# Optimization experiments

Measured on AMD Instinct MI355X. Metric: run time of the kernel, lower is better.

The kernel has to match this reference:

```python
import jax, jax.numpy as jnp
import numpy as np

B, T, C = 128, 256, 384
H, HD = 8, 48          # num_heads, head_dim
WINDOW = 64

def setup_inputs() -> dict:
    key = jax.random.key(0)
    ks = jax.random.split(key, 5)
    return {
        "x": jax.random.normal(ks[0], (B, T, C), dtype=jnp.float32),
        "W_qkv": jax.random.normal(ks[1], (C, 3 * C), dtype=jnp.float32) * (1.0 / np.sqrt(C)),
        "b_qkv": jax.random.normal(ks[2], (3 * C,), dtype=jnp.float32) * 0.02,
        "W_proj": jax.random.normal(ks[3], (C, C), dtype=jnp.float32) * (1.0 / np.sqrt(C)),
        "b_proj": jax.random.normal(ks[4], (C,), dtype=jnp.float32) * 0.02,
        "gate": jnp.ones((C,), dtype=jnp.float32),
    }

def reference(x, W_qkv, b_qkv, W_proj, b_proj, gate):
    Bx, Tx, Cx = x.shape
    qkv = x @ W_qkv + b_qkv                                   # [B,T,3C]
    q, k, v = jnp.split(qkv, 3, axis=-1)
    q = q.reshape(Bx, Tx, H, HD).transpose(0, 2, 1, 3)        # [B,H,T,hd]
    k = k.reshape(Bx, Tx, H, HD).transpose(0, 2, 1, 3)
    v = v.reshape(Bx, Tx, H, HD).transpose(0, 2, 1, 3)
    scale = 1.0 / np.sqrt(HD).astype(np.float32)
    att = jnp.einsum("bhqd,bhkd->bhqk", q, k) * scale        # [B,H,T,T]
    idx = jnp.arange(Tx)
    causal = idx[:, None] >= idx[None, :]                     # lower-tri
    local = jnp.abs(idx[None, :] - idx[:, None]) <= WINDOW
    mask = (causal & local)[None, None, :, :]
    att = jnp.where(mask, att, -jnp.inf)
    att = jax.nn.softmax(att, axis=-1)
    out = jnp.einsum("bhqk,bhkd->bhqd", att, v)               # [B,H,T,hd]
    out = out.transpose(0, 2, 1, 3).reshape(Bx, Tx, Cx)       # [B,T,C]
    return (out * gate) @ W_proj + b_proj
```

## Files before the change

### kernel.cpp

```cpp
#include <hip/hip_runtime.h>
#include <hip/hip_bf16.h>

typedef __attribute__((ext_vector_type(8))) short bf16x8;
typedef __attribute__((ext_vector_type(4))) float floatx4;

#define NB 128
#define NT 256
#define NC 384
#define NH 8
#define ND 48
#define CPLANE (128 * 8 * 256 * 48)

static __device__ __forceinline__ unsigned short f2bf(float f) {
  __hip_bfloat16 h = __float2bfloat16(f);
  return __builtin_bit_cast(unsigned short, h);
}

static __device__ __forceinline__ void gload16(const unsigned short* g, unsigned short* l) {
  __builtin_amdgcn_global_load_lds(
      (const __attribute__((address_space(1))) void*)g,
      (__attribute__((address_space(3))) void*)l, 16, 0, 0);
}

__global__ __launch_bounds__(256) void k_prep(const float* __restrict__ x,
                                              const float* __restrict__ Wq,
                                              const float* __restrict__ Wp,
                                              const float* __restrict__ gate,
                                              unsigned short* __restrict__ xbf,
                                              unsigned short* __restrict__ WqT,
                                              unsigned short* __restrict__ WpT) {
  const int blk = blockIdx.x;
  const int t = threadIdx.x;
  if (blk < 144) {
    __shared__ float T[64][65];
    const float* src;
    unsigned short* dst;
    int N, kt, nt;
    const bool isWp = (blk >= 108);
    if (!isWp) { src = Wq; dst = WqT; N = 1152; kt = blk / 18; nt = blk % 18; }
    else { int b2 = blk - 108; src = Wp; dst = WpT; N = 384; kt = b2 / 6; nt = b2 % 6; }
    const int k0 = kt * 64, n0 = nt * 64;
    const int r = t >> 2, c = (t & 3) * 16;
    const float* s = src + (size_t)(k0 + r) * N + n0 + c;
#pragma unroll
    for (int i = 0; i < 4; ++i) *(float4*)&T[r][c + i * 4] = ((const float4*)s)[i];
    __syncthreads();
    float gv[16];
    if (isWp) {
#pragma unroll
      for (int i = 0; i < 4; ++i) *(float4*)&gv[i * 4] = ((const float4*)(gate + k0 + c))[i];
    } else {
#pragma unroll
      for (int i = 0; i < 16; ++i) gv[i] = 1.f;
    }
    unsigned short o[16];
#pragma unroll
    for (int i = 0; i < 16; ++i) o[i] = f2bf(T[c + i][r] * gv[i]);
    unsigned short* dp = dst + (size_t)(n0 + r) * 384 + k0 + c;
    *(bf16x8*)dp = *(bf16x8*)&o[0];
    *(bf16x8*)(dp + 8) = *(bf16x8*)&o[8];
  } else {
    const int n8 = (NB * NT * NC) / 8;
    int idx = (blk - 144) * 256 + t;
    const int stride = (gridDim.x - 144) * 256;
    for (; idx < n8; idx += stride) {
      const float* s = x + (size_t)idx * 8;
      float v[8];
      *(float4*)&v[0] = ((const float4*)s)[0];
      *(float4*)&v[4] = ((const float4*)s)[1];
      bf16x8 p;
#pragma unroll
      for (int i = 0; i < 8; ++i) p[i] = f2bf(v[i]);
      *(bf16x8*)(xbf + (size_t)idx * 8) = p;
    }
  }
}

#define STAGE_G(Ag, Bg, k0, buf)                                                     \
  {                                                                                  \
    const int r0_ = (lane >> 2), sw0_ = 8 * ((lane & 3) ^ ((r0_ >> 1) & 3));         \
    const int r1_ = r0_ + 16,    sw1_ = 8 * ((lane & 3) ^ ((r1_ >> 1) & 3));         \
    gload16((Ag) + (size_t)r0_ * 384 + (k0) + sw0_, As + (buf)*4096 + (w * 32) * 32);  \
    gload16((Ag) + (size_t)r1_ * 384 + (k0) + sw1_, As + (buf)*4096 + (w * 32 + 16) * 32); \
    gload16((Bg) + (size_t)r0_ * 384 + (k0) + sw0_, Bs + (buf)*4096 + (w * 32) * 32);  \
    gload16((Bg) + (size_t)r1_ * 384 + (k0) + sw1_, Bs + (buf)*4096 + (w * 32 + 16) * 32); \
  }

#define GEMM_PIPE(Ag, Bg)                                                            \
  STAGE_G(Ag, Bg, 0, 0);                                                             \
  STAGE_G(Ag, Bg, 32, 1);                                                            \
  _Pragma("unroll") for (int t_ = 0; t_ < 12; ++t_) {                                \
    if (t_ < 11) asm volatile("s_waitcnt vmcnt(4)" ::: "memory");                    \
    else         asm volatile("s_waitcnt vmcnt(0)" ::: "memory");                    \
    __builtin_amdgcn_s_barrier();                                                    \
    if (t_ < 10) STAGE_G(Ag, Bg, (t_ + 2) * 32, (t_ + 2) % 3);                       \
    const unsigned short* Ac_ = As + (t_ % 3) * 4096;                                \
    const unsigned short* Bc_ = Bs + (t_ % 3) * 4096;                                \
    bf16x8 a_[4], b_[4];                                                             \
    _Pragma("unroll") for (int mt = 0; mt < 4; ++mt) {                               \
      const int R = wm * 64 + mt * 16 + lq;                                          \
      a_[mt] = *(const bf16x8*)&Ac_[R * 32 + 8 * (lg ^ ((R >> 1) & 3))];             \
    }                                                                                \
    _Pragma("unroll") for (int nt = 0; nt < 4; ++nt) {                               \
      const int R = wn * 64 + nt * 16 + lq;                                          \
      b_[nt] = *(const bf16x8*)&Bc_[R * 32 + 8 * (lg ^ ((R >> 1) & 3))];             \
    }                                                                                \
    _Pragma("unroll") for (int mt = 0; mt < 4; ++mt)                                 \
      _Pragma("unroll") for (int nt = 0; nt < 4; ++nt)                               \
        acc[mt][nt] = __builtin_amdgcn_mfma_f32_16x16x32_bf16(a_[mt], b_[nt], acc[mt][nt], 0, 0, 0); \
  }

__global__ __launch_bounds__(256) void k_qkv(const unsigned short* __restrict__ xb,
                                             const unsigned short* __restrict__ WqT,
                                             const float* __restrict__ bq,
                                             unsigned short* __restrict__ qkv) {
  __shared__ __align__(16) unsigned short As[3 * 4096];
  __shared__ __align__(16) unsigned short Bs[3 * 4096];
  const int t = threadIdx.x, lane = t & 63, w = t >> 6;
  const int wm = w >> 1, wn = w & 1;
  const int lq = lane & 15, lg = lane >> 4;
  const int swz = (blockIdx.x & 7) * 288 + (blockIdx.x >> 3);
  const int m0 = (swz / 9) * 128, n0 = (swz % 9) * 128;
  const int comp = n0 / 384;
  const unsigned short* Ag = xb + (size_t)(m0 + w * 32) * 384;
  const unsigned short* Bg = WqT + (size_t)(n0 + w * 32) * 384;
  floatx4 acc[4][4] = {};

  GEMM_PIPE(Ag, Bg);

  __builtin_amdgcn_s_barrier();
  unsigned short* Ew = ((w < 2) ? As : Bs) + 2 * 4096 + (w & 1) * 2048;
#pragma unroll
  for (int p = 0; p < 4; ++p) {
#pragma unroll
    for (int nt = 0; nt < 4; ++nt) {
      const float bias = bq[n0 + wn * 64 + nt * 16 + lq];
#pragma unroll
      for (int j = 0; j < 4; ++j)
        Ew[(lg * 4 + j) * 72 + nt * 16 + lq] = f2bf(acc[p][nt][j] + bias);
    }
    asm volatile("s_waitcnt lgkmcnt(0)" ::: "memory");
    __builtin_amdgcn_sched_barrier(0);
#pragma unroll
    for (int cc = 0; cc < 2; ++cc) {
      const int c = cc * 64 + lane;
      const int r16 = c >> 3, k8 = c & 7;
      bf16x8 v = *(const bf16x8*)&Ew[r16 * 72 + k8 * 8];
      const int lc = n0 - comp * 384 + wn * 64 + k8 * 8;
      const int hh = lc / 48, d0 = lc - hh * 48;
      const int R = m0 + wm * 64 + p * 16 + r16;
      *(bf16x8*)(qkv + (size_t)comp * CPLANE +
                 (((size_t)((R >> 8) * 8 + hh) * 256 + (R & 255)) * 48 + d0)) = v;
    }
    asm volatile("s_waitcnt lgkmcnt(0)" ::: "memory");
    __builtin_amdgcn_sched_barrier(0);
  }
}

__global__ __launch_bounds__(256) void k_proj(const unsigned short* __restrict__ A,
                                              const unsigned short* __restrict__ WpT,
                                              const float* __restrict__ bp,
                                              float* __restrict__ out) {
  __shared__ __align__(16) unsigned short As[3 * 4096];
  __shared__ __align__(16) unsigned short Bs[3 * 4096];
  const int t = threadIdx.x, lane = t & 63, w = t >> 6;
  const int wm = w >> 1, wn = w & 1;
  const int lq = lane & 15, lg = lane >> 4;
  const int swz = (blockIdx.x & 7) * 96 + (blockIdx.x >> 3);
  const int m0 = (swz / 3) * 128, n0 = (swz % 3) * 128;
  const unsigned short* Ag = A + (size_t)(m0 + w * 32) * 384;
  const unsigned short* Bg = WpT + (size_t)(n0 + w * 32) * 384;
  floatx4 acc[4][4] = {};

  GEMM_PIPE(Ag, Bg);

#pragma unroll
  for (int nt = 0; nt < 4; ++nt) {
    const int col = n0 + wn * 64 + nt * 16 + lq;
    const float bias = bp[col];
#pragma unroll
    for (int mt = 0; mt < 4; ++mt)
#pragma unroll
      for (int j = 0; j < 4; ++j) {
        const int row = m0 + wm * 64 + mt * 16 + lg * 4 + j;
        out[(size_t)row * 384 + col] = acc[mt][nt][j] + bias;
      }
  }
}

__global__ __launch_bounds__(256) void k_attn(const unsigned short* __restrict__ qkv,
                                              unsigned short* __restrict__ attg) {
  __shared__ __align__(16) unsigned short Ks[256 * 72];
  __shared__ __align__(16) unsigned short Vt[48 * 280];
  __shared__ __align__(16) unsigned short Ps[4 * 16 * 104];
  const int t = threadIdx.x;
  const int bh = blockIdx.x;
  const int b = bh >> 3, h = bh & 7;
  const size_t kvoff = (size_t)bh * NT * ND;
  const unsigned short* qptr = qkv + kvoff;
  const unsigned short* kptr = qkv + (size_t)CPLANE + kvoff;
  const unsigned short* vptr = qkv + (size_t)2 * CPLANE + kvoff;

  {
    const unsigned short* src = kptr + (size_t)t * ND;
    unsigned short* dst = &Ks[t * 72];
#pragma unroll
    for (int i = 0; i < 6; ++i) *(bf16x8*)(dst + i * 8) = *(const bf16x8*)(src + i * 8);
    bf16x8 z = {};
    *(bf16x8*)(dst + 48) = z;
    *(bf16x8*)(dst + 56) = z;
  }
  {
    const unsigned short* src = vptr + (size_t)t * ND;
    bf16x8 vv[6];
#pragma unroll
    for (int i = 0; i < 6; ++i) vv[i] = *(const bf16x8*)(src + i * 8);
#pragma unroll
    for (int i = 0; i < 6; ++i)
#pragma unroll
      for (int j = 0; j < 8; ++j)
        Vt[(i * 8 + j) * 280 + t] = (unsigned short)vv[i][j];
  }
  if (t < 144) {
    bf16x8 z = {};
    *(bf16x8*)&Vt[(t / 3) * 280 + 256 + (t % 3) * 8] = z;
  }
  __syncthreads();

  const int lane = t & 63, w = t >> 6;
  const int lq = lane & 15, lg = lane >> 4;
  const float scale = 0.14433756729740643f;
  unsigned short* pw = &Ps[w * 16 * 104];

  for (int s = 0; s < 4; ++s) {
    const int qs = s * 64 + w * 16;
    const int kstart = (qs >= 64) ? (qs - 64) : 0;

    const unsigned short* qrow = qptr + (size_t)(qs + lq) * ND;
    bf16x8 aq0 = *(const bf16x8*)(qrow + lg * 8);
    bf16x8 aq1 = {};
    if (lg < 2) aq1 = *(const bf16x8*)(qrow + 32 + lg * 8);

    floatx4 sv4[5];
#pragma unroll
    for (int kt = 0; kt < 5; ++kt) {
      const unsigned short* kr = &Ks[(kstart + kt * 16 + lq) * 72];
      bf16x8 kb0 = *(const bf16x8*)(kr + lg * 8);
      bf16x8 kb1 = *(const bf16x8*)(kr + 32 + lg * 8);
      floatx4 z = {};
      z = __builtin_amdgcn_mfma_f32_16x16x32_bf16(aq0, kb0, z, 0, 0, 0);
      z = __builtin_amdgcn_mfma_f32_16x16x32_bf16(aq1, kb1, z, 0, 0, 0);
      sv4[kt] = z;
    }

    floatx4 pj[5];
#pragma unroll
    for (int j = 0; j < 4; ++j) {
      const int qa = qs + lg * 4 + j;
      float mx = -1e30f;
      float sv[5];
      bool ok[5];
#pragma unroll
      for (int kt = 0; kt < 5; ++kt) {
        const int ka = kstart + kt * 16 + lq;
        sv[kt] = sv4[kt][j] * scale;
        ok[kt] = (ka <= qa) && (qa - ka <= 64);
        if (ok[kt]) mx = fmaxf(mx, sv[kt]);
      }
#pragma unroll
      for (int dd = 1; dd < 16; dd <<= 1) mx = fmaxf(mx, __shfl_xor(mx, dd));
      float sum = 0.f;
#pragma unroll
      for (int kt = 0; kt < 5; ++kt) {
        float p = ok[kt] ? __expf(sv[kt] - mx) : 0.f;
        pj[kt][j] = p;
        sum += p;
      }
#pragma unroll
      for (int dd = 1; dd < 16; dd <<= 1) sum += __shfl_xor(sum, dd);
      const float inv = 1.f / sum;
#pragma unroll
      for (int kt = 0; kt < 5; ++kt) pj[kt][j] *= inv;
    }

#pragma unroll
    for (int kt = 0; kt < 5; ++kt)
#pragma unroll
      for (int j = 0; j < 4; ++j)
        pw[(lg * 4 + j) * 104 + kt * 16 + lq] = f2bf(pj[kt][j]);
#pragma unroll
    for (int j = 0; j < 4; ++j) pw[lq * 104 + 80 + lg * 4 + j] = 0;

    floatx4 o[3] = {};
#pragma unroll
    for (int c = 0; c < 3; ++c) {
      bf16x8 ap = *(const bf16x8*)&pw[lq * 104 + c * 32 + lg * 8];
#pragma unroll
      for (int nt = 0; nt < 3; ++nt) {
        bf16x8 av = *(const bf16x8*)&Vt[(nt * 16 + lq) * 280 + kstart + c * 32 + lg * 8];
        o[nt] = __builtin_amdgcn_mfma_f32_16x16x32_bf16(ap, av, o[nt], 0, 0, 0);
      }
    }
#pragma unroll
    for (int nt = 0; nt < 3; ++nt) {
      const int d = nt * 16 + lq;
      const int c = h * ND + d;
#pragma unroll
      for (int j = 0; j < 4; ++j) {
        const int tt = qs + lg * 4 + j;
        attg[((size_t)b * NT + tt) * NC + c] = f2bf(o[nt][j]);
      }
    }
    __syncthreads();
  }
}

extern "C" void kernel_launch(void* const* d_in, const int* in_sizes, int n_in,
                              void* d_out, int out_size, void* d_ws, size_t ws_size,
                              hipStream_t stream) {
  const float* x    = (const float*)d_in[0];
  const float* Wq   = (const float*)d_in[1];
  const float* bq   = (const float*)d_in[2];
  const float* Wp   = (const float*)d_in[3];
  const float* bp   = (const float*)d_in[4];
  const float* gate = (const float*)d_in[5];

  const size_t nx = (size_t)NB * NT * NC;
  unsigned short* attg = (unsigned short*)d_ws;
  unsigned short* xbf  = attg + nx;
  unsigned short* qkvp = xbf + nx;
  unsigned short* WqT  = qkvp + (size_t)3 * CPLANE;
  unsigned short* WpT  = WqT + (size_t)384 * 1152;
  float* out = (float*)d_out;

  k_prep<<<dim3(1680), 256, 0, stream>>>(x, Wq, Wp, gate, xbf, WqT, WpT);
  k_qkv<<<dim3(2304), 256, 0, stream>>>(xbf, WqT, bq, qkvp);
  k_attn<<<dim3(1024), 256, 0, stream>>>(qkvp, attg);
  k_proj<<<dim3(768), 256, 0, stream>>>(attg, WpT, bp, out);
}
```

Before: 110.9 us.

## Enlarge QKV and projection GEMM tiles to 256x128 with eight waves

```diff
diff --git a/kernel.cpp b/kernel.cpp
--- a/kernel.cpp
+++ b/kernel.cpp
@@ -76,26 +76,26 @@
   }
 }
 
-#define STAGE_G(Ag, Bg, k0, buf)                                                     \
+#define STAGE_G5(Ag, Bg, k0, buf)                                                    \
   {                                                                                  \
-    const int r0_ = (lane >> 2), sw0_ = 8 * ((lane & 3) ^ ((r0_ >> 1) & 3));         \
-    const int r1_ = r0_ + 16,    sw1_ = 8 * ((lane & 3) ^ ((r1_ >> 1) & 3));         \
-    gload16((Ag) + (size_t)r0_ * 384 + (k0) + sw0_, As + (buf)*4096 + (w * 32) * 32);  \
-    gload16((Ag) + (size_t)r1_ * 384 + (k0) + sw1_, As + (buf)*4096 + (w * 32 + 16) * 32); \
-    gload16((Bg) + (size_t)r0_ * 384 + (k0) + sw0_, Bs + (buf)*4096 + (w * 32) * 32);  \
-    gload16((Bg) + (size_t)r1_ * 384 + (k0) + sw1_, Bs + (buf)*4096 + (w * 32 + 16) * 32); \
-  }
-
-#define GEMM_PIPE(Ag, Bg)                                                            \
-  STAGE_G(Ag, Bg, 0, 0);                                                             \
-  STAGE_G(Ag, Bg, 32, 1);                                                            \
-  _Pragma("unroll") for (int t_ = 0; t_ < 12; ++t_) {                                \
-    if (t_ < 11) asm volatile("s_waitcnt vmcnt(4)" ::: "memory");                    \
-    else         asm volatile("s_waitcnt vmcnt(0)" ::: "memory");                    \
-    __builtin_amdgcn_s_barrier();                                                    \
-    if (t_ < 10) STAGE_G(Ag, Bg, (t_ + 2) * 32, (t_ + 2) % 3);                       \
-    const unsigned short* Ac_ = As + (t_ % 3) * 4096;                                \
-    const unsigned short* Bc_ = Bs + (t_ % 3) * 4096;                                \
+    const int ra0_ = w * 32 + (lane >> 2);                                           \
+    const int ra1_ = ra0_ + 16;                                                      \
+    const int rb_  = w * 16 + (lane >> 2);                                           \
+    gload16((Ag) + (size_t)ra0_ * 384 + (k0) + 8 * ((lane & 3) ^ ((ra0_ >> 1) & 3)), \
+            As + (buf)*8192 + (w * 32) * 32);                                        \
+    gload16((Ag) + (size_t)ra1_ * 384 + (k0) + 8 * ((lane & 3) ^ ((ra1_ >> 1) & 3)), \
+            As + (buf)*8192 + (w * 32 + 16) * 32);                                   \
+    gload16((Bg) + (size_t)rb_ * 384 + (k0) + 8 * ((lane & 3) ^ ((rb_ >> 1) & 3)),   \
+            Bs + (buf)*4096 + (w * 16) * 32);                                        \
+  }
+
+#define QITER5(vmstr, gmod3, STG)                                                    \
+  asm volatile("s_waitcnt vmcnt(" vmstr ")" ::: "memory");                           \
+  __builtin_amdgcn_s_barrier();                                                      \
+  STG;                                                                               \
+  {                                                                                  \
+    const unsigned short* Ac_ = As + (gmod3) * 8192;                                 \
+    const unsigned short* Bc_ = Bs + (gmod3) * 4096;                                 \
     bf16x8 a_[4], b_[4];                                                             \
     _Pragma("unroll") for (int mt = 0; mt < 4; ++mt) {                               \
       const int R = wm * 64 + mt * 16 + lq;                                          \
@@ -110,26 +110,42 @@
         acc[mt][nt] = __builtin_amdgcn_mfma_f32_16x16x32_bf16(a_[mt], b_[nt], acc[mt][nt], 0, 0, 0); \
   }
 
-__global__ __launch_bounds__(256) void k_qkv(const unsigned short* __restrict__ xb,
+#define GEMM_PIPE5(Ag, Bg)                                                           \
+  STAGE_G5(Ag, Bg, 0, 0);                                                            \
+  STAGE_G5(Ag, Bg, 32, 1);                                                           \
+  QITER5("3", 0, STAGE_G5(Ag, Bg, 64, 2));                                           \
+  QITER5("3", 1, STAGE_G5(Ag, Bg, 96, 0));                                           \
+  QITER5("3", 2, STAGE_G5(Ag, Bg, 128, 1));                                          \
+  QITER5("3", 0, STAGE_G5(Ag, Bg, 160, 2));                                          \
+  QITER5("3", 1, STAGE_G5(Ag, Bg, 192, 0));                                          \
+  QITER5("3", 2, STAGE_G5(Ag, Bg, 224, 1));                                          \
+  QITER5("3", 0, STAGE_G5(Ag, Bg, 256, 2));                                          \
+  QITER5("3", 1, STAGE_G5(Ag, Bg, 288, 0));                                          \
+  QITER5("3", 2, STAGE_G5(Ag, Bg, 320, 1));                                          \
+  QITER5("3", 0, STAGE_G5(Ag, Bg, 352, 2));                                          \
+  QITER5("3", 1, {});                                                                \
+  QITER5("0", 2, {});
+
+__global__ __launch_bounds__(512) void k_qkv(const unsigned short* __restrict__ xb,
                                              const unsigned short* __restrict__ WqT,
                                              const float* __restrict__ bq,
                                              unsigned short* __restrict__ qkv) {
-  __shared__ __align__(16) unsigned short As[3 * 4096];
+  __shared__ __align__(16) unsigned short As[3 * 8192];
   __shared__ __align__(16) unsigned short Bs[3 * 4096];
   const int t = threadIdx.x, lane = t & 63, w = t >> 6;
   const int wm = w >> 1, wn = w & 1;
   const int lq = lane & 15, lg = lane >> 4;
-  const int swz = (blockIdx.x & 7) * 288 + (blockIdx.x >> 3);
-  const int m0 = (swz / 9) * 128, n0 = (swz % 9) * 128;
+  const int swz = (blockIdx.x & 7) * 144 + (blockIdx.x >> 3);
+  const int m0 = (swz / 9) * 256, n0 = (swz % 9) * 128;
   const int comp = n0 / 384;
-  const unsigned short* Ag = xb + (size_t)(m0 + w * 32) * 384;
-  const unsigned short* Bg = WqT + (size_t)(n0 + w * 32) * 384;
+  const unsigned short* Ag = xb + (size_t)m0 * 384;
+  const unsigned short* Bg = WqT + (size_t)n0 * 384;
   floatx4 acc[4][4] = {};
 
-  GEMM_PIPE(Ag, Bg);
+  GEMM_PIPE5(Ag, Bg);
 
   __builtin_amdgcn_s_barrier();
-  unsigned short* Ew = ((w < 2) ? As : Bs) + 2 * 4096 + (w & 1) * 2048;
+  unsigned short* Ew = As + w * 2048;
 #pragma unroll
   for (int p = 0; p < 4; ++p) {
 #pragma unroll
@@ -157,22 +173,22 @@
   }
 }
 
-__global__ __launch_bounds__(256) void k_proj(const unsigned short* __restrict__ A,
+__global__ __launch_bounds__(512) void k_proj(const unsigned short* __restrict__ A,
                                               const unsigned short* __restrict__ WpT,
                                               const float* __restrict__ bp,
                                               float* __restrict__ out) {
-  __shared__ __align__(16) unsigned short As[3 * 4096];
+  __shared__ __align__(16) unsigned short As[3 * 8192];
   __shared__ __align__(16) unsigned short Bs[3 * 4096];
   const int t = threadIdx.x, lane = t & 63, w = t >> 6;
   const int wm = w >> 1, wn = w & 1;
   const int lq = lane & 15, lg = lane >> 4;
-  const int swz = (blockIdx.x & 7) * 96 + (blockIdx.x >> 3);
-  const int m0 = (swz / 3) * 128, n0 = (swz % 3) * 128;
-  const unsigned short* Ag = A + (size_t)(m0 + w * 32) * 384;
-  const unsigned short* Bg = WpT + (size_t)(n0 + w * 32) * 384;
+  const int swz = (blockIdx.x & 7) * 48 + (blockIdx.x >> 3);
+  const int m0 = (swz / 3) * 256, n0 = (swz % 3) * 128;
+  const unsigned short* Ag = A + (size_t)m0 * 384;
+  const unsigned short* Bg = WpT + (size_t)n0 * 384;
   floatx4 acc[4][4] = {};
 
-  GEMM_PIPE(Ag, Bg);
+  GEMM_PIPE5(Ag, Bg);
 
 #pragma unroll
   for (int nt = 0; nt < 4; ++nt) {
@@ -334,7 +350,7 @@
   float* out = (float*)d_out;
 
   k_prep<<<dim3(1680), 256, 0, stream>>>(x, Wq, Wp, gate, xbf, WqT, WpT);
-  k_qkv<<<dim3(2304), 256, 0, stream>>>(xbf, WqT, bq, qkvp);
+  k_qkv<<<dim3(1152), 512, 0, stream>>>(xbf, WqT, bq, qkvp);
   k_attn<<<dim3(1024), 256, 0, stream>>>(qkvp, attg);
-  k_proj<<<dim3(768), 256, 0, stream>>>(attg, WpT, bp, out);
-}
+  k_proj<<<dim3(384), 512, 0, stream>>>(attg, WpT, bp, out);
+}
```

Result: no change. 112.8 us (+1.7%).

## Fuse x fp32-to-bf16 conversion into QKV GEMM A-tile loads

Applied to the files above, without the earlier changes.

```diff
diff --git a/kernel.cpp b/kernel.cpp
--- a/kernel.cpp
+++ b/kernel.cpp
@@ -22,57 +22,146 @@
       (__attribute__((address_space(3))) void*)l, 16, 0, 0);
 }
 
-__global__ __launch_bounds__(256) void k_prep(const float* __restrict__ x,
-                                              const float* __restrict__ Wq,
+static __device__ __forceinline__ void gload16f(const float* g, float* l) {
+  __builtin_amdgcn_global_load_lds(
+      (const __attribute__((address_space(1))) void*)g,
+      (__attribute__((address_space(3))) void*)l, 16, 0, 0);
+}
+
+__global__ __launch_bounds__(256) void k_prep(const float* __restrict__ Wq,
                                               const float* __restrict__ Wp,
                                               const float* __restrict__ gate,
-                                              unsigned short* __restrict__ xbf,
                                               unsigned short* __restrict__ WqT,
                                               unsigned short* __restrict__ WpT) {
   const int blk = blockIdx.x;
   const int t = threadIdx.x;
-  if (blk < 144) {
-    __shared__ float T[64][65];
-    const float* src;
-    unsigned short* dst;
-    int N, kt, nt;
-    const bool isWp = (blk >= 108);
-    if (!isWp) { src = Wq; dst = WqT; N = 1152; kt = blk / 18; nt = blk % 18; }
-    else { int b2 = blk - 108; src = Wp; dst = WpT; N = 384; kt = b2 / 6; nt = b2 % 6; }
-    const int k0 = kt * 64, n0 = nt * 64;
-    const int r = t >> 2, c = (t & 3) * 16;
-    const float* s = src + (size_t)(k0 + r) * N + n0 + c;
-#pragma unroll
-    for (int i = 0; i < 4; ++i) *(float4*)&T[r][c + i * 4] = ((const float4*)s)[i];
-    __syncthreads();
-    float gv[16];
-    if (isWp) {
-#pragma unroll
-      for (int i = 0; i < 4; ++i) *(float4*)&gv[i * 4] = ((const float4*)(gate + k0 + c))[i];
-    } else {
-#pragma unroll
-      for (int i = 0; i < 16; ++i) gv[i] = 1.f;
-    }
-    unsigned short o[16];
-#pragma unroll
-    for (int i = 0; i < 16; ++i) o[i] = f2bf(T[c + i][r] * gv[i]);
-    unsigned short* dp = dst + (size_t)(n0 + r) * 384 + k0 + c;
-    *(bf16x8*)dp = *(bf16x8*)&o[0];
-    *(bf16x8*)(dp + 8) = *(bf16x8*)&o[8];
+  __shared__ float T[64][65];
+  const float* src;
+  unsigned short* dst;
+  int N, kt, nt;
+  const bool isWp = (blk >= 108);
+  if (!isWp) { src = Wq; dst = WqT; N = 1152; kt = blk / 18; nt = blk % 18; }
+  else { int b2 = blk - 108; src = Wp; dst = WpT; N = 384; kt = b2 / 6; nt = b2 % 6; }
+  const int k0 = kt * 64, n0 = nt * 64;
+  const int r = t >> 2, c = (t & 3) * 16;
+  const float* s = src + (size_t)(k0 + r) * N + n0 + c;
+#pragma unroll
+  for (int i = 0; i < 4; ++i) *(float4*)&T[r][c + i * 4] = ((const float4*)s)[i];
+  __syncthreads();
+  float gv[16];
+  if (isWp) {
+#pragma unroll
+    for (int i = 0; i < 4; ++i) *(float4*)&gv[i * 4] = ((const float4*)(gate + k0 + c))[i];
   } else {
-    const int n8 = (NB * NT * NC) / 8;
-    int idx = (blk - 144) * 256 + t;
-    const int stride = (gridDim.x - 144) * 256;
-    for (; idx < n8; idx += stride) {
-      const float* s = x + (size_t)idx * 8;
-      float v[8];
-      *(float4*)&v[0] = ((const float4*)s)[0];
-      *(float4*)&v[4] = ((const float4*)s)[1];
-      bf16x8 p;
-#pragma unroll
-      for (int i = 0; i < 8; ++i) p[i] = f2bf(v[i]);
-      *(bf16x8*)(xbf + (size_t)idx * 8) = p;
-    }
+#pragma unroll
+    for (int i = 0; i < 16; ++i) gv[i] = 1.f;
+  }
+  unsigned short o[16];
+#pragma unroll
+  for (int i = 0; i < 16; ++i) o[i] = f2bf(T[c + i][r] * gv[i]);
+  unsigned short* dp = dst + (size_t)(n0 + r) * 384 + k0 + c;
+  *(bf16x8*)dp = *(bf16x8*)&o[0];
+  *(bf16x8*)(dp + 8) = *(bf16x8*)&o[8];
+}
+
+#define STAGE_QF(k0, buf)                                                            \
+  {                                                                                  \
+    _Pragma("unroll") for (int l_ = 0; l_ < 4; ++l_) {                               \
+      const int cid_ = l_ * 256 + t;                                                 \
+      const int row_ = cid_ >> 3, kc_ = cid_ & 7;                                    \
+      const int kcs_ = kc_ ^ (row_ & 7);                                             \
+      gload16f(xg + (size_t)(m0 + row_) * 384 + (k0) + kcs_ * 4,                     \
+               Asf + (buf) * 4096 + (l_ * 256 + w * 64) * 4);                        \
+    }                                                                                \
+    {                                                                                \
+      const int r0_ = w * 32 + (lane >> 2), sw0_ = 8 * ((lane & 3) ^ ((r0_ >> 1) & 3)); \
+      const int r1_ = r0_ + 16, sw1_ = 8 * ((lane & 3) ^ ((r1_ >> 1) & 3));          \
+      gload16(Bg + (size_t)r0_ * 384 + (k0) + sw0_, Bs + (buf)*4096 + (w * 32) * 32);  \
+      gload16(Bg + (size_t)r1_ * 384 + (k0) + sw1_, Bs + (buf)*4096 + (w * 32 + 16) * 32); \
+    }                                                                                \
+  }
+
+#define QITER_QF(vmstr, gmod3, STG)                                                  \
+  asm volatile("s_waitcnt vmcnt(" vmstr ")" ::: "memory");                           \
+  __builtin_amdgcn_s_barrier();                                                      \
+  STG;                                                                               \
+  {                                                                                  \
+    const float* Af_ = Asf + (gmod3) * 4096;                                         \
+    const unsigned short* Bc_ = Bs + (gmod3) * 4096;                                 \
+    bf16x8 a_[4], b_[4];                                                             \
+    _Pragma("unroll") for (int mt = 0; mt < 4; ++mt) {                               \
+      const int R = wm * 64 + mt * 16 + lq;                                          \
+      float f_[8];                                                                   \
+      *(float4*)&f_[0] = *(const float4*)&Af_[R * 32 + ((2 * lg) ^ (R & 7)) * 4];    \
+      *(float4*)&f_[4] = *(const float4*)&Af_[R * 32 + ((2 * lg + 1) ^ (R & 7)) * 4]; \
+      _Pragma("unroll") for (int e_ = 0; e_ < 8; ++e_)                               \
+        a_[mt][e_] = (short)f2bf(f_[e_]);                                            \
+    }                                                                                \
+    _Pragma("unroll") for (int nt = 0; nt < 4; ++nt) {                               \
+      const int R = wn * 64 + nt * 16 + lq;                                          \
+      b_[nt] = *(const bf16x8*)&Bc_[R * 32 + 8 * (lg ^ ((R >> 1) & 3))];             \
+    }                                                                                \
+    _Pragma("unroll") for (int mt = 0; mt < 4; ++mt)                                 \
+      _Pragma("unroll") for (int nt = 0; nt < 4; ++nt)                               \
+        acc[mt][nt] = __builtin_amdgcn_mfma_f32_16x16x32_bf16(a_[mt], b_[nt], acc[mt][nt], 0, 0, 0); \
+  }
+
+__global__ __launch_bounds__(256) void k_qkv(const float* __restrict__ xg,
+                                             const unsigned short* __restrict__ WqT,
+                                             const float* __restrict__ bq,
+                                             unsigned short* __restrict__ qkv) {
+  __shared__ __align__(16) float Asf[3 * 4096];
+  __shared__ __align__(16) unsigned short Bs[3 * 4096];
+  const int t = threadIdx.x, lane = t & 63, w = t >> 6;
+  const int wm = w >> 1, wn = w & 1;
+  const int lq = lane & 15, lg = lane >> 4;
+  const int swz = (blockIdx.x & 7) * 288 + (blockIdx.x >> 3);
+  const int m0 = (swz / 9) * 128, n0 = (swz % 9) * 128;
+  const int comp = n0 / 384;
+  const unsigned short* Bg = WqT + (size_t)n0 * 384;
+  floatx4 acc[4][4] = {};
+
+  STAGE_QF(0, 0);
+  STAGE_QF(32, 1);
+  QITER_QF("6", 0, STAGE_QF(64, 2));
+  QITER_QF("6", 1, STAGE_QF(96, 0));
+  QITER_QF("6", 2, STAGE_QF(128, 1));
+  QITER_QF("6", 0, STAGE_QF(160, 2));
+  QITER_QF("6", 1, STAGE_QF(192, 0));
+  QITER_QF("6", 2, STAGE_QF(224, 1));
+  QITER_QF("6", 0, STAGE_QF(256, 2));
+  QITER_QF("6", 1, STAGE_QF(288, 0));
+  QITER_QF("6", 2, STAGE_QF(320, 1));
+  QITER_QF("6", 0, STAGE_QF(352, 2));
+  QITER_QF("6", 1, {});
+  QITER_QF("0", 2, {});
+
+  __builtin_amdgcn_s_barrier();
+  unsigned short* Ew = Bs + w * 2048;
+#pragma unroll
+  for (int p = 0; p < 4; ++p) {
+#pragma unroll
+    for (int nt = 0; nt < 4; ++nt) {
+      const float bias = bq[n0 + wn * 64 + nt * 16 + lq];
+#pragma unroll
+      for (int j = 0; j < 4; ++j)
+        Ew[(lg * 4 + j) * 72 + nt * 16 + lq] = f2bf(acc[p][nt][j] + bias);
+    }
+    asm volatile("s_waitcnt lgkmcnt(0)" ::: "memory");
+    __builtin_amdgcn_sched_barrier(0);
+#pragma unroll
+    for (int cc = 0; cc < 2; ++cc) {
+      const int c = cc * 64 + lane;
+      const int r16 = c >> 3, k8 = c & 7;
+      bf16x8 v = *(const bf16x8*)&Ew[r16 * 72 + k8 * 8];
+      const int lc = n0 - comp * 384 + wn * 64 + k8 * 8;
+      const int hh = lc / 48, d0 = lc - hh * 48;
+      const int R = m0 + wm * 64 + p * 16 + r16;
+      *(bf16x8*)(qkv + (size_t)comp * CPLANE +
+                 (((size_t)((R >> 8) * 8 + hh) * 256 + (R & 255)) * 48 + d0)) = v;
+    }
+    asm volatile("s_waitcnt lgkmcnt(0)" ::: "memory");
+    __builtin_amdgcn_sched_barrier(0);
   }
 }
 
@@ -110,53 +199,6 @@
         acc[mt][nt] = __builtin_amdgcn_mfma_f32_16x16x32_bf16(a_[mt], b_[nt], acc[mt][nt], 0, 0, 0); \
   }
 
-__global__ __launch_bounds__(256) void k_qkv(const unsigned short* __restrict__ xb,
-                                             const unsigned short* __restrict__ WqT,
-                                             const float* __restrict__ bq,
-                                             unsigned short* __restrict__ qkv) {
-  __shared__ __align__(16) unsigned short As[3 * 4096];
-  __shared__ __align__(16) unsigned short Bs[3 * 4096];
-  const int t = threadIdx.x, lane = t & 63, w = t >> 6;
-  const int wm = w >> 1, wn = w & 1;
-  const int lq = lane & 15, lg = lane >> 4;
-  const int swz = (blockIdx.x & 7) * 288 + (blockIdx.x >> 3);
-  const int m0 = (swz / 9) * 128, n0 = (swz % 9) * 128;
-  const int comp = n0 / 384;
-  const unsigned short* Ag = xb + (size_t)(m0 + w * 32) * 384;
-  const unsigned short* Bg = WqT + (size_t)(n0 + w * 32) * 384;
-  floatx4 acc[4][4] = {};
-
-  GEMM_PIPE(Ag, Bg);
-
-  __builtin_amdgcn_s_barrier();
-  unsigned short* Ew = ((w < 2) ? As : Bs) + 2 * 4096 + (w & 1) * 2048;
-#pragma unroll
-  for (int p = 0; p < 4; ++p) {
-#pragma unroll
-    for (int nt = 0; nt < 4; ++nt) {
-      const float bias = bq[n0 + wn * 64 + nt * 16 + lq];
-#pragma unroll
-      for (int j = 0; j < 4; ++j)
-        Ew[(lg * 4 + j) * 72 + nt * 16 + lq] = f2bf(acc[p][nt][j] + bias);
-    }
-    asm volatile("s_waitcnt lgkmcnt(0)" ::: "memory");
-    __builtin_amdgcn_sched_barrier(0);
-#pragma unroll
-    for (int cc = 0; cc < 2; ++cc) {
-      const int c = cc * 64 + lane;
-      const int r16 = c >> 3, k8 = c & 7;
-      bf16x8 v = *(const bf16x8*)&Ew[r16 * 72 + k8 * 8];
-      const int lc = n0 - comp * 384 + wn * 64 + k8 * 8;
-      const int hh = lc / 48, d0 = lc - hh * 48;
-      const int R = m0 + wm * 64 + p * 16 + r16;
-      *(bf16x8*)(qkv + (size_t)comp * CPLANE +
-                 (((size_t)((R >> 8) * 8 + hh) * 256 + (R & 255)) * 48 + d0)) = v;
-    }
-    asm volatile("s_waitcnt lgkmcnt(0)" ::: "memory");
-    __builtin_amdgcn_sched_barrier(0);
-  }
-}
-
 __global__ __launch_bounds__(256) void k_proj(const unsigned short* __restrict__ A,
                                               const unsigned short* __restrict__ WpT,
                                               const float* __restrict__ bp,
@@ -327,14 +369,13 @@
 
   const size_t nx = (size_t)NB * NT * NC;
   unsigned short* attg = (unsigned short*)d_ws;
-  unsigned short* xbf  = attg + nx;
-  unsigned short* qkvp = xbf + nx;
+  unsigned short* qkvp = attg + nx;
   unsigned short* WqT  = qkvp + (size_t)3 * CPLANE;
   unsigned short* WpT  = WqT + (size_t)384 * 1152;
   float* out = (float*)d_out;
 
-  k_prep<<<dim3(1680), 256, 0, stream>>>(x, Wq, Wp, gate, xbf, WqT, WpT);
-  k_qkv<<<dim3(2304), 256, 0, stream>>>(xbf, WqT, bq, qkvp);
+  k_prep<<<dim3(144), 256, 0, stream>>>(Wq, Wp, gate, WqT, WpT);
+  k_qkv<<<dim3(2304), 256, 0, stream>>>(x, WqT, bq, qkvp);
   k_attn<<<dim3(1024), 256, 0, stream>>>(qkvp, attg);
   k_proj<<<dim3(768), 256, 0, stream>>>(attg, WpT, bp, out);
 }
```

Result: slower. 115.2 us (+3.8%).
